# Kernel optimization log

Hardware: AMD Instinct MI355X
Metric: run time of the kernel (lower is better)

Reference implementation:

```python
import math
import jax, jax.numpy as jnp
import numpy as np

N_HEADS, INPUT_DIM, EMBED_DIM = 8, 512, 512
KEY_DIM = EMBED_DIM // N_HEADS  # 64, val_dim == key_dim
BATCH, N = 4, 2048


def setup_inputs() -> dict:
    key = jax.random.key(0)
    ks = jax.random.split(key, 6)
    def unif(k, shape):
        stdv = 1.0 / math.sqrt(shape[-1])
        return jax.random.uniform(k, shape, jnp.float32, -stdv, stdv)
    q = jax.random.normal(ks[0], (BATCH, N, INPUT_DIM), jnp.float32)
    mask = jax.random.randint(ks[1], (BATCH, N, N), 0, 2, jnp.int32)
    W_query = unif(ks[2], (N_HEADS, INPUT_DIM, KEY_DIM))
    W_key = unif(ks[3], (N_HEADS, INPUT_DIM, KEY_DIM))
    W_val = unif(ks[4], (N_HEADS, INPUT_DIM, KEY_DIM))
    W_out = unif(ks[5], (N_HEADS, KEY_DIM, EMBED_DIM))
    return {"q": q, "mask": mask, "W_query": W_query, "W_key": W_key,
            "W_val": W_val, "W_out": W_out}


def reference(q, mask, W_query, W_key, W_val, W_out):
    # Self-attention: k is None, v is None -> k = q, v = q (module forward_).
    norm = 1.0 / math.sqrt(KEY_DIM)
    m = mask.astype(bool)[None]  # (1, b, nq, ng) broadcast over heads
    Q = jnp.einsum('bnd,hdk->hbnk', q, W_query)  # (h, b, nq, dk)
    K = jnp.einsum('bnd,hdk->hbnk', q, W_key)    # (h, b, ng, dk)
    V = jnp.einsum('bnd,hdv->hbnv', q, W_val)    # (h, b, ng, dv)
    scores = norm * jnp.einsum('hbqk,hbgk->hbqg', Q, K)  # (h, b, nq, ng)
    scores = jnp.where(m, -jnp.inf, scores)
    attn = jax.nn.softmax(scores, axis=-1)
    attn = jnp.where(m, 0.0, attn)  # zero out masked (also kills NaN rows)
    heads = jnp.einsum('hbqg,hbgv->hbqv', attn, V)
    out = jnp.einsum('hbqv,hve->bqe', heads, W_out)  # (b, nq, embed)
    return out
```

## Files before the change

kernel.cpp:

```cpp
#include <hip/hip_runtime.h>
#include <hip/hip_bf16.h>
#include <stdint.h>

using bf16 = __hip_bfloat16;
typedef __attribute__((ext_vector_type(8))) short short8;
typedef __attribute__((ext_vector_type(4))) short short4b;
typedef __attribute__((ext_vector_type(4))) float f32x4;
typedef __attribute__((ext_vector_type(4))) unsigned int u32x4;

#if __has_builtin(__builtin_amdgcn_exp2f)
#define EXP2(x) __builtin_amdgcn_exp2f(x)
#else
#define EXP2(x) exp2f(x)
#endif

__device__ __forceinline__ short8 load8(const bf16* p) {
  return *reinterpret_cast<const short8*>(p);
}
__device__ __forceinline__ short4b load4(const bf16* p) {
  return *reinterpret_cast<const short4b*>(p);
}
__device__ __forceinline__ short f2b(float f) {
  return __builtin_bit_cast(short, __float2bfloat16(f));
}
__device__ __forceinline__ unsigned int pk2(float a, float b) {
  return (unsigned int)(unsigned short)f2b(a) |
         ((unsigned int)(unsigned short)f2b(b) << 16);
}
__device__ __forceinline__ void asy16(const bf16* g, bf16* l) {
  __builtin_amdgcn_global_load_lds(
      (const __attribute__((address_space(1))) void*)g,
      (__attribute__((address_space(3))) void*)l, 16, 0, 0);
}

__global__ void k_prep(const float4* __restrict__ x, ushort4* __restrict__ xb,
                       const float* __restrict__ Wq, const float* __restrict__ Wk,
                       const float* __restrict__ Wv, const float* __restrict__ Wo,
                       bf16* __restrict__ Wcat, bf16* __restrict__ Wot,
                       const int4* __restrict__ m4,
                       unsigned long long* __restrict__ bits) {
  int blk = blockIdx.x;
  if (blk < 4096) {
    int i = blk * 256 + threadIdx.x;
    float4 v = x[i];
    ushort4 o;
    o.x = (unsigned short)f2b(v.x);
    o.y = (unsigned short)f2b(v.y);
    o.z = (unsigned short)f2b(v.z);
    o.w = (unsigned short)f2b(v.w);
    xb[i] = o;
  } else if (blk < 8192) {
    int t = (blk - 4096) * 256 + threadIdx.x;
    if (t < 786432) {
      int rr = t >> 9, d = t & 511;
      int which = rr >> 9;
      int hdk = rr & 511, h = hdk >> 6, dk = hdk & 63;
      const float* W = (which == 0) ? Wq : ((which == 1) ? Wk : Wv);
      float v = W[(h * 512 + d) * 64 + dk];
      if (which == 0) v *= 0.18033688011112042f;
      Wcat[t] = __float2bfloat16(v);
    } else {
      int u = t - 786432;
      int e = u >> 9, hv = u & 511;
      Wot[u] = __float2bfloat16(Wo[hv * 512 + e]);
    }
  } else {
    int i = (blk - 8192) * 256 + threadIdx.x;
    int4 v = m4[i];
    unsigned int nib = (unsigned)(v.x != 0) | ((unsigned)(v.y != 0) << 1) |
                       ((unsigned)(v.z != 0) << 2) | ((unsigned)(v.w != 0) << 3);
    unsigned long long w = (unsigned long long)nib << (4 * (threadIdx.x & 15));
    w |= __shfl_xor(w, 1);
    w |= __shfl_xor(w, 2);
    w |= __shfl_xor(w, 4);
    w |= __shfl_xor(w, 8);
    if ((threadIdx.x & 15) == 0) bits[i >> 4] = w;
  }
}

__device__ __forceinline__ void gemm128(const bf16* __restrict__ A,
                                        const bf16* __restrict__ Bt,
                                        bf16* As, bf16* Bs,
                                        int rowBase, int colBase,
                                        f32x4 acc[4][4]) {
  const int tid = threadIdx.x;
  const int lane = tid & 63, w = tid >> 6;
  const int g = lane >> 4, r = lane & 15;

  auto stage = [&](int buf, int s) {
#pragma unroll
    for (int p = 0; p < 4; ++p) {
      int c = p * 256 + tid;
      int row = c >> 3, w8 = c & 7, sg = w8 ^ (row & 7);
      asy16(A + (size_t)(rowBase + row) * 512 + s * 64 + sg * 8,
            As + buf * 8192 + c * 8);
    }
#pragma unroll
    for (int p = 0; p < 4; ++p) {
      int c = p * 256 + tid;
      int row = c >> 3, w8 = c & 7, sg = w8 ^ (row & 7);
      asy16(Bt + (size_t)(colBase + row) * 512 + s * 64 + sg * 8,
            Bs + buf * 8192 + c * 8);
    }
  };

  stage(0, 0);
  int buf = 0;
  const int rbl = (w >> 1) * 64, cbl = (w & 1) * 64;
  for (int s = 0; s < 8; ++s) {
    __syncthreads();
    if (s < 7) stage(buf ^ 1, s + 1);
    const bf16* a0 = As + buf * 8192;
    const bf16* b0 = Bs + buf * 8192;
#pragma unroll
    for (int kk = 0; kk < 2; ++kk) {
      short8 af[4], bfr[4];
#pragma unroll
      for (int mt = 0; mt < 4; ++mt) {
        int row = rbl + mt * 16 + r;
        af[mt] = load8(a0 + (row * 8 + ((kk * 4 + g) ^ (row & 7))) * 8);
      }
#pragma unroll
      for (int nt = 0; nt < 4; ++nt) {
        int col = cbl + nt * 16 + r;
        bfr[nt] = load8(b0 + (col * 8 + ((kk * 4 + g) ^ (col & 7))) * 8);
      }
#pragma unroll
      for (int mt = 0; mt < 4; ++mt)
#pragma unroll
        for (int nt = 0; nt < 4; ++nt)
          acc[mt][nt] = __builtin_amdgcn_mfma_f32_16x16x32_bf16(
              af[mt], bfr[nt], acc[mt][nt], 0, 0, 0);
    }
    buf ^= 1;
  }
}

__global__ __launch_bounds__(256, 2) void k_proj_qkv(
    const bf16* __restrict__ Xb, const bf16* __restrict__ Wcat,
    bf16* __restrict__ Qb, bf16* __restrict__ Kb, bf16* __restrict__ Vt) {
  __shared__ __align__(16) bf16 As[2 * 8192];
  __shared__ __align__(16) bf16 Bs[2 * 8192];
  int rowBase = blockIdx.x * 128, colBase = blockIdx.y * 128;
  f32x4 acc[4][4] = {};
  gemm128(Xb, Wcat, As, Bs, rowBase, colBase, acc);
  const int lane = threadIdx.x & 63, w = threadIdx.x >> 6;
  const int g = lane >> 4, r = lane & 15;
#pragma unroll
  for (int mt = 0; mt < 4; ++mt) {
    int row0 = rowBase + (w >> 1) * 64 + mt * 16 + 4 * g;
    int b = row0 >> 11, n0 = row0 & 2047;
#pragma unroll
    for (int nt = 0; nt < 4; ++nt) {
      int col = colBase + (w & 1) * 64 + nt * 16 + r;
      if (col < 1024) {
        bf16* dst = (col < 512) ? Qb : Kb;
        int hh = (col >> 6) & 7, dk = col & 63;
        bf16* p0 = dst + ((size_t)(b * 8 + hh) * 2048 + n0) * 64 + dk;
#pragma unroll
        for (int rr = 0; rr < 4; ++rr)
          p0[rr * 64] = __float2bfloat16(acc[mt][nt][rr]);
      } else {
        int hdv = col - 1024;
        short4b pkv;
#pragma unroll
        for (int rr = 0; rr < 4; ++rr) pkv[rr] = f2b(acc[mt][nt][rr]);
        *reinterpret_cast<short4b*>(Vt + ((size_t)b * 512 + hdv) * 2048 + n0) = pkv;
      }
    }
  }
}

__global__ __launch_bounds__(256, 2) void k_proj_out(
    const bf16* __restrict__ O, const bf16* __restrict__ Wot,
    float* __restrict__ out) {
  __shared__ __align__(16) bf16 As[2 * 8192];
  __shared__ __align__(16) bf16 Bs[2 * 8192];
  int rowBase = blockIdx.x * 128, colBase = blockIdx.y * 128;
  f32x4 acc[4][4] = {};
  gemm128(O, Wot, As, Bs, rowBase, colBase, acc);
  const int lane = threadIdx.x & 63, w = threadIdx.x >> 6;
  const int g = lane >> 4, r = lane & 15;
#pragma unroll
  for (int mt = 0; mt < 4; ++mt) {
    int row0 = rowBase + (w >> 1) * 64 + mt * 16 + 4 * g;
#pragma unroll
    for (int nt = 0; nt < 4; ++nt) {
      int col = colBase + (w & 1) * 64 + nt * 16 + r;
#pragma unroll
      for (int rr = 0; rr < 4; ++rr)
        out[(size_t)(row0 + rr) * 512 + col] = acc[mt][nt][rr];
    }
  }
}

__global__ __launch_bounds__(256, 4) void k_attn(const bf16* __restrict__ Q,
    const bf16* __restrict__ K, const bf16* __restrict__ Vt,
    const unsigned long long* __restrict__ MB, bf16* __restrict__ O) {
  const int blin = blockIdx.x;
  const int j = blin >> 3;
  const int bh = (blin & 7) * 4 + (j >> 5);
  const int qt = j & 31;
  const int b = bh >> 3, h = bh & 7;
  const int tid = threadIdx.x;
  const int lane = tid & 63;
  const int wave = tid >> 6;
  const int g = lane >> 4, r = lane & 15;
  const int rx = r & 7;
  const int qbase = qt * 64 + wave * 16;

  __shared__ __align__(16) bf16 Kl[2][64 * 64];
  __shared__ __align__(16) bf16 Vl[2][64 * 64];

  const bf16* Kp = K + (size_t)bh * 2048 * 64;
  const bf16* Vp = Vt + (size_t)bh * 64 * 2048;

  const bf16* Qp = Q + ((size_t)bh * 2048 + qbase + r) * 64;
  short8 qf0 = load8(Qp + g * 8);
  short8 qf1 = load8(Qp + 32 + g * 8);
  const unsigned long long* Mp = MB + ((size_t)b * 2048 + qbase + r) * 32;

  short8 ones;
#pragma unroll
  for (int i = 0; i < 8; ++i) ones[i] = (short)0x3F80;

  f32x4 acc[4] = {};
  f32x4 acc_l = {};

  auto stage = [&](int buf, int kt) {
    const bf16* Kg = Kp + kt * 4096;
    const bf16* Vg = Vp + kt * 64;
#pragma unroll
    for (int p = 0; p < 2; ++p) {
      int c = p * 256 + tid;
      int row = c >> 3, gr = c & 7, sg = gr ^ (row & 7);
      asy16(Kg + row * 64 + sg * 8, &Kl[buf][0] + c * 8);
    }
#pragma unroll
    for (int p = 0; p < 2; ++p) {
      int c = p * 256 + tid;
      int row = c >> 3, gr = c & 7, sg = gr ^ (row & 7);
      asy16(Vg + (size_t)row * 2048 + sg * 8, &Vl[buf][0] + c * 8);
    }
  };

  stage(0, 0);
  int buf = 0;

  for (int kt = 0; kt < 32; ++kt) {
    __syncthreads();
    if (kt < 31) stage(buf ^ 1, kt + 1);

    unsigned long long mw = Mp[kt];
    const bf16* kl = &Kl[buf][0];
    const bf16* vl = &Vl[buf][0];

    f32x4 st[4];
#pragma unroll
    for (int kc = 0; kc < 4; ++kc) {
      const bf16* krow = kl + (kc * 16 + r) * 64;
      short8 kf0 = load8(krow + ((g) ^ rx) * 8);
      short8 kf1 = load8(krow + ((4 + g) ^ rx) * 8);
      f32x4 z = {};
      z = __builtin_amdgcn_mfma_f32_16x16x32_bf16(kf0, qf0, z, 0, 0, 0);
      st[kc] = __builtin_amdgcn_mfma_f32_16x16x32_bf16(kf1, qf1, z, 0, 0, 0);
    }

    unsigned ml = (unsigned)mw >> (4 * g);
    unsigned mh = (unsigned)(mw >> 32) >> (4 * g);
    float p[16];
#pragma unroll
    for (int kc = 0; kc < 4; ++kc)
#pragma unroll
      for (int rr = 0; rr < 4; ++rr) {
        float e = EXP2(st[kc][rr]);
        unsigned wsel = (kc & 2) ? mh : ml;
        bool bad = (wsel >> (((kc & 1) << 4) + rr)) & 1u;
        p[kc * 4 + rr] = bad ? 0.f : e;
      }
    u32x4 q0, q1;
#pragma unroll
    for (int i2 = 0; i2 < 4; ++i2) {
      q0[i2] = pk2(p[2 * i2], p[2 * i2 + 1]);
      q1[i2] = pk2(p[8 + 2 * i2], p[8 + 2 * i2 + 1]);
    }
    short8 pa0 = __builtin_bit_cast(short8, q0);
    short8 pa1 = __builtin_bit_cast(short8, q1);

    acc_l = __builtin_amdgcn_mfma_f32_16x16x32_bf16(pa0, ones, acc_l, 0, 0, 0);
    acc_l = __builtin_amdgcn_mfma_f32_16x16x32_bf16(pa1, ones, acc_l, 0, 0, 0);

#pragma unroll
    for (int dvs = 0; dvs < 4; ++dvs) {
      const bf16* vrow = vl + (dvs * 16 + r) * 64 + (g & 1) * 4;
      short4b v0 = load4(vrow + (((g >> 1)) ^ rx) * 8);
      short4b v1 = load4(vrow + ((2 + (g >> 1)) ^ rx) * 8);
      short4b v2 = load4(vrow + ((4 + (g >> 1)) ^ rx) * 8);
      short4b v3 = load4(vrow + ((6 + (g >> 1)) ^ rx) * 8);
      short8 vb0 = {v0[0], v0[1], v0[2], v0[3], v1[0], v1[1], v1[2], v1[3]};
      short8 vb1 = {v2[0], v2[1], v2[2], v2[3], v3[0], v3[1], v3[2], v3[3]};
      acc[dvs] = __builtin_amdgcn_mfma_f32_16x16x32_bf16(pa0, vb0, acc[dvs], 0, 0, 0);
      acc[dvs] = __builtin_amdgcn_mfma_f32_16x16x32_bf16(pa1, vb1, acc[dvs], 0, 0, 0);
    }
    buf ^= 1;
  }

  float inv[4];
#pragma unroll
  for (int rr = 0; rr < 4; ++rr)
    inv[rr] = (acc_l[rr] > 0.f) ? 1.f / acc_l[rr] : 0.f;
  bf16* Op = O + ((size_t)b * 2048 + qbase + 4 * g) * 512 + h * 64;
#pragma unroll
  for (int dvs = 0; dvs < 4; ++dvs)
#pragma unroll
    for (int rr = 0; rr < 4; ++rr)
      Op[rr * 512 + dvs * 16 + r] = __float2bfloat16(acc[dvs][rr] * inv[rr]);
}


extern "C" void kernel_launch(void* const* d_in, const int* in_sizes, int n_in,
                              void* d_out, int out_size, void* d_ws, size_t ws_size,
                              hipStream_t stream) {
  const float* q    = (const float*)d_in[0];
  const int*   mask = (const int*)d_in[1];
  const float* Wq   = (const float*)d_in[2];
  const float* Wk   = (const float*)d_in[3];
  const float* Wv   = (const float*)d_in[4];
  const float* Wo   = (const float*)d_in[5];
  float* out = (float*)d_out;

  char* ws = (char*)d_ws;
  const size_t MB1 = 1024 * 1024;
  bf16* Xb   = (bf16*)(ws + 0);
  bf16* Qb   = (bf16*)(ws + 8 * MB1);
  bf16* Kb   = (bf16*)(ws + 16 * MB1);
  bf16* Vtb  = (bf16*)(ws + 24 * MB1);
  bf16* Ob   = (bf16*)(ws + 32 * MB1);
  unsigned long long* Mbits = (unsigned long long*)(ws + 40 * MB1);
  bf16* Wcat = (bf16*)(ws + 42 * MB1);
  bf16* Wot  = (bf16*)(ws + 42 * MB1 + 1536 * 512 * 2);

  k_prep<<<24576, 256, 0, stream>>>((const float4*)q, (ushort4*)Xb,
                                    Wq, Wk, Wv, Wo, Wcat, Wot,
                                    (const int4*)mask, Mbits);
  k_proj_qkv<<<dim3(64, 12), 256, 0, stream>>>(Xb, Wcat, Qb, Kb, Vtb);
  k_attn<<<1024, 256, 0, stream>>>(Qb, Kb, Vtb, Mbits, Ob);
  k_proj_out<<<dim3(64, 4), 256, 0, stream>>>(Ob, Wot, out);
}
```

Measured before the change: 223.7 us.

## Process two query sub-tiles per wave with triple-buffered K/V and software-pipelined QK

Each wave now handles 32 query rows, as two 16-row sub-tiles, instead of 16. This halves the grid to 512 blocks and reuses each K/V LDS fragment for twice as many MFMAs. K/V staging moves to a three-buffer ring, and the QK^T scores for the next key tile are computed before the softmax/PV of the current tile so MFMA work overlaps with exp and mask processing. The cost is higher register pressure (launch bounds lowered to 2 blocks per SM), more LDS per block, and fewer blocks to fill the 256 CUs.

```diff
diff --git a/kernel.cpp b/kernel.cpp
--- a/kernel.cpp
+++ b/kernel.cpp
@@ -194,38 +194,43 @@
   }
 }
 
-__global__ __launch_bounds__(256, 4) void k_attn(const bf16* __restrict__ Q,
+__global__ __launch_bounds__(256, 2) void k_attn(const bf16* __restrict__ Q,
     const bf16* __restrict__ K, const bf16* __restrict__ Vt,
     const unsigned long long* __restrict__ MB, bf16* __restrict__ O) {
   const int blin = blockIdx.x;
   const int j = blin >> 3;
-  const int bh = (blin & 7) * 4 + (j >> 5);
-  const int qt = j & 31;
+  const int bh = (blin & 7) * 4 + (j >> 4);
+  const int qt = j & 15;
   const int b = bh >> 3, h = bh & 7;
   const int tid = threadIdx.x;
   const int lane = tid & 63;
   const int wave = tid >> 6;
   const int g = lane >> 4, r = lane & 15;
   const int rx = r & 7;
-  const int qbase = qt * 64 + wave * 16;
-
-  __shared__ __align__(16) bf16 Kl[2][64 * 64];
-  __shared__ __align__(16) bf16 Vl[2][64 * 64];
+  const int qbase = qt * 128 + wave * 32;
+
+  __shared__ __align__(16) bf16 Kl[3][64 * 64];
+  __shared__ __align__(16) bf16 Vl[3][64 * 64];
 
   const bf16* Kp = K + (size_t)bh * 2048 * 64;
   const bf16* Vp = Vt + (size_t)bh * 64 * 2048;
 
-  const bf16* Qp = Q + ((size_t)bh * 2048 + qbase + r) * 64;
-  short8 qf0 = load8(Qp + g * 8);
-  short8 qf1 = load8(Qp + 32 + g * 8);
-  const unsigned long long* Mp = MB + ((size_t)b * 2048 + qbase + r) * 32;
+  short8 qf[2][2];
+#pragma unroll
+  for (int s = 0; s < 2; ++s) {
+    const bf16* Qp = Q + ((size_t)bh * 2048 + qbase + s * 16 + r) * 64;
+    qf[s][0] = load8(Qp + g * 8);
+    qf[s][1] = load8(Qp + 32 + g * 8);
+  }
+  const unsigned long long* Mp0 = MB + ((size_t)b * 2048 + qbase + r) * 32;
+  const unsigned long long* Mp1 = MB + ((size_t)b * 2048 + qbase + 16 + r) * 32;
 
   short8 ones;
 #pragma unroll
   for (int i = 0; i < 8; ++i) ones[i] = (short)0x3F80;
 
-  f32x4 acc[4] = {};
-  f32x4 acc_l = {};
+  f32x4 acc[2][4] = {};
+  f32x4 acc_l[2] = {};
 
   auto stage = [&](int buf, int kt) {
     const bf16* Kg = Kp + kt * 4096;
@@ -244,52 +249,68 @@
     }
   };
 
-  stage(0, 0);
-  int buf = 0;
-
-  for (int kt = 0; kt < 32; ++kt) {
-    __syncthreads();
-    if (kt < 31) stage(buf ^ 1, kt + 1);
-
-    unsigned long long mw = Mp[kt];
-    const bf16* kl = &Kl[buf][0];
-    const bf16* vl = &Vl[buf][0];
-
-    f32x4 st[4];
+  auto qk = [&](const bf16* kl, f32x4 stl[4][2]) {
 #pragma unroll
     for (int kc = 0; kc < 4; ++kc) {
       const bf16* krow = kl + (kc * 16 + r) * 64;
       short8 kf0 = load8(krow + ((g) ^ rx) * 8);
       short8 kf1 = load8(krow + ((4 + g) ^ rx) * 8);
-      f32x4 z = {};
-      z = __builtin_amdgcn_mfma_f32_16x16x32_bf16(kf0, qf0, z, 0, 0, 0);
-      st[kc] = __builtin_amdgcn_mfma_f32_16x16x32_bf16(kf1, qf1, z, 0, 0, 0);
-    }
-
-    unsigned ml = (unsigned)mw >> (4 * g);
-    unsigned mh = (unsigned)(mw >> 32) >> (4 * g);
-    float p[16];
-#pragma unroll
-    for (int kc = 0; kc < 4; ++kc)
-#pragma unroll
-      for (int rr = 0; rr < 4; ++rr) {
-        float e = EXP2(st[kc][rr]);
-        unsigned wsel = (kc & 2) ? mh : ml;
-        bool bad = (wsel >> (((kc & 1) << 4) + rr)) & 1u;
-        p[kc * 4 + rr] = bad ? 0.f : e;
-      }
-    u32x4 q0, q1;
-#pragma unroll
-    for (int i2 = 0; i2 < 4; ++i2) {
-      q0[i2] = pk2(p[2 * i2], p[2 * i2 + 1]);
-      q1[i2] = pk2(p[8 + 2 * i2], p[8 + 2 * i2 + 1]);
-    }
-    short8 pa0 = __builtin_bit_cast(short8, q0);
-    short8 pa1 = __builtin_bit_cast(short8, q1);
-
-    acc_l = __builtin_amdgcn_mfma_f32_16x16x32_bf16(pa0, ones, acc_l, 0, 0, 0);
-    acc_l = __builtin_amdgcn_mfma_f32_16x16x32_bf16(pa1, ones, acc_l, 0, 0, 0);
-
+      f32x4 z0 = {};
+      z0 = __builtin_amdgcn_mfma_f32_16x16x32_bf16(kf0, qf[0][0], z0, 0, 0, 0);
+      stl[kc][0] = __builtin_amdgcn_mfma_f32_16x16x32_bf16(kf1, qf[0][1], z0, 0, 0, 0);
+      f32x4 z1 = {};
+      z1 = __builtin_amdgcn_mfma_f32_16x16x32_bf16(kf0, qf[1][0], z1, 0, 0, 0);
+      stl[kc][1] = __builtin_amdgcn_mfma_f32_16x16x32_bf16(kf1, qf[1][1], z1, 0, 0, 0);
+    }
+  };
+
+  stage(0, 0);
+  stage(1, 1);
+  unsigned long long mw0c = Mp0[0], mw1c = Mp1[0];
+  __syncthreads();
+  f32x4 st_cur[4][2];
+  qk(&Kl[0][0], st_cur);
+
+  int b_cur = 0, b_nxt = 1, b_st = 2;
+
+  for (int kt = 0; kt < 32; ++kt) {
+    __syncthreads();
+    if (kt < 30) stage(b_st, kt + 2);
+    unsigned long long mw0n = 0, mw1n = 0;
+    if (kt < 31) { mw0n = Mp0[kt + 1]; mw1n = Mp1[kt + 1]; }
+
+    f32x4 stn[4][2];
+    if (kt < 31) qk(&Kl[b_nxt][0], stn);
+
+    short8 pa[2][2];
+#pragma unroll
+    for (int s = 0; s < 2; ++s) {
+      unsigned long long mw = s ? mw1c : mw0c;
+      unsigned ml = (unsigned)mw >> (4 * g);
+      unsigned mh = (unsigned)(mw >> 32) >> (4 * g);
+      float p[16];
+#pragma unroll
+      for (int kc = 0; kc < 4; ++kc)
+#pragma unroll
+        for (int rr = 0; rr < 4; ++rr) {
+          float e = EXP2(st_cur[kc][s][rr]);
+          unsigned wsel = (kc & 2) ? mh : ml;
+          bool bad = (wsel >> (((kc & 1) << 4) + rr)) & 1u;
+          p[kc * 4 + rr] = bad ? 0.f : e;
+        }
+      u32x4 q0, q1;
+#pragma unroll
+      for (int i2 = 0; i2 < 4; ++i2) {
+        q0[i2] = pk2(p[2 * i2], p[2 * i2 + 1]);
+        q1[i2] = pk2(p[8 + 2 * i2], p[8 + 2 * i2 + 1]);
+      }
+      pa[s][0] = __builtin_bit_cast(short8, q0);
+      pa[s][1] = __builtin_bit_cast(short8, q1);
+      acc_l[s] = __builtin_amdgcn_mfma_f32_16x16x32_bf16(pa[s][0], ones, acc_l[s], 0, 0, 0);
+      acc_l[s] = __builtin_amdgcn_mfma_f32_16x16x32_bf16(pa[s][1], ones, acc_l[s], 0, 0, 0);
+    }
+
+    const bf16* vl = &Vl[b_cur][0];
 #pragma unroll
     for (int dvs = 0; dvs < 4; ++dvs) {
       const bf16* vrow = vl + (dvs * 16 + r) * 64 + (g & 1) * 4;
@@ -299,22 +320,36 @@
       short4b v3 = load4(vrow + ((6 + (g >> 1)) ^ rx) * 8);
       short8 vb0 = {v0[0], v0[1], v0[2], v0[3], v1[0], v1[1], v1[2], v1[3]};
       short8 vb1 = {v2[0], v2[1], v2[2], v2[3], v3[0], v3[1], v3[2], v3[3]};
-      acc[dvs] = __builtin_amdgcn_mfma_f32_16x16x32_bf16(pa0, vb0, acc[dvs], 0, 0, 0);
-      acc[dvs] = __builtin_amdgcn_mfma_f32_16x16x32_bf16(pa1, vb1, acc[dvs], 0, 0, 0);
-    }
-    buf ^= 1;
-  }
-
-  float inv[4];
-#pragma unroll
-  for (int rr = 0; rr < 4; ++rr)
-    inv[rr] = (acc_l[rr] > 0.f) ? 1.f / acc_l[rr] : 0.f;
-  bf16* Op = O + ((size_t)b * 2048 + qbase + 4 * g) * 512 + h * 64;
-#pragma unroll
-  for (int dvs = 0; dvs < 4; ++dvs)
+#pragma unroll
+      for (int s = 0; s < 2; ++s) {
+        acc[s][dvs] = __builtin_amdgcn_mfma_f32_16x16x32_bf16(pa[s][0], vb0, acc[s][dvs], 0, 0, 0);
+        acc[s][dvs] = __builtin_amdgcn_mfma_f32_16x16x32_bf16(pa[s][1], vb1, acc[s][dvs], 0, 0, 0);
+      }
+    }
+
+#pragma unroll
+    for (int kc = 0; kc < 4; ++kc) {
+      st_cur[kc][0] = stn[kc][0];
+      st_cur[kc][1] = stn[kc][1];
+    }
+    mw0c = mw0n;
+    mw1c = mw1n;
+    int t = b_cur; b_cur = b_nxt; b_nxt = b_st; b_st = t;
+  }
+
+#pragma unroll
+  for (int s = 0; s < 2; ++s) {
+    float inv[4];
 #pragma unroll
     for (int rr = 0; rr < 4; ++rr)
-      Op[rr * 512 + dvs * 16 + r] = __float2bfloat16(acc[dvs][rr] * inv[rr]);
+      inv[rr] = (acc_l[s][rr] > 0.f) ? 1.f / acc_l[s][rr] : 0.f;
+    bf16* Op = O + ((size_t)b * 2048 + qbase + s * 16 + 4 * g) * 512 + h * 64;
+#pragma unroll
+    for (int dvs = 0; dvs < 4; ++dvs)
+#pragma unroll
+      for (int rr = 0; rr < 4; ++rr)
+        Op[rr * 512 + dvs * 16 + r] = __float2bfloat16(acc[s][dvs][rr] * inv[rr]);
+  }
 }
 
 
@@ -344,6 +379,6 @@
                                     Wq, Wk, Wv, Wo, Wcat, Wot,
                                     (const int4*)mask, Mbits);
   k_proj_qkv<<<dim3(64, 12), 256, 0, stream>>>(Xb, Wcat, Qb, Kb, Vtb);
-  k_attn<<<1024, 256, 0, stream>>>(Qb, Kb, Vtb, Mbits, Ob);
+  k_attn<<<512, 256, 0, stream>>>(Qb, Kb, Vtb, Mbits, Ob);
   k_proj_out<<<dim3(64, 4), 256, 0, stream>>>(Ob, Wot, out);
 }
```

Measured after the change: 216.7 us. 3.1% less time.
